# Performance work log

Hardware: AMD Instinct MI355X
Metric: run time of the kernel (lower is better)

## Reference

```python
import jax, jax.numpy as jnp
import numpy as np

N = 100000
E = 800000
D_IN = 64
D_HID = 64
D_OUT = 47


def gcn_conv(x, edge_index, W, b):
    # GCNConv with normalize=False: linear transform then sum-aggregate over edges.
    h = x @ W                              # [N, d_out]
    src, dst = edge_index[0], edge_index[1]
    msg = h[src]                           # [E, d_out] gather
    agg = jax.ops.segment_sum(msg, dst, num_segments=N)  # [N, d_out] scatter-add
    return agg + b


def setup_inputs() -> dict:
    key = jax.random.key(0)
    ks = jax.random.split(key, 8)
    x = jax.random.normal(ks[0], (N, D_IN), dtype=jnp.float32)
    edge_index = jax.random.randint(ks[1], (2, E), 0, N, dtype=jnp.int64)
    # Glorot-ish init for weights, zeros for bias (as in GCNConv.reset_parameters)
    def glorot(k, fan_in, fan_out):
        s = jnp.sqrt(6.0 / (fan_in + fan_out))
        return jax.random.uniform(k, (fan_in, fan_out), jnp.float32, -s, s)
    W1 = glorot(ks[2], D_IN, D_HID)
    b1 = jnp.zeros((D_HID,), jnp.float32)
    W2 = glorot(ks[3], D_HID, D_HID)
    b2 = jnp.zeros((D_HID,), jnp.float32)
    W3 = glorot(ks[4], D_HID, D_OUT)
    b3 = jnp.zeros((D_OUT,), jnp.float32)
    return {"x": x, "edge_index": edge_index,
            "W1": W1, "b1": b1, "W2": W2, "b2": b2, "W3": W3, "b3": b3}


def reference(x, edge_index, W1, b1, W2, b2, W3, b3):
    # Layer 1: conv -> relu (dropout is identity at inference)
    h = jax.nn.relu(gcn_conv(x, edge_index, W1, b1))
    # Layer 2
    h = jax.nn.relu(gcn_conv(h, edge_index, W2, b2))
    # Output layer + log_softmax over classes
    out = gcn_conv(h, edge_index, W3, b3)
    return jax.nn.log_softmax(out, axis=-1)
```

## Files before the change

kernel.cpp:

```cpp
#include <hip/hip_runtime.h>
#include <cmath>


#define B1_EPB 4096
#define BKT_SH 8
#define CHUNK  256
#define PSTRIDE 512

typedef __attribute__((ext_vector_type(8))) short bf8;
typedef __attribute__((ext_vector_type(4))) float f4;

__device__ __forceinline__ unsigned int f2bf(float x) {
  unsigned int u = __float_as_uint(x);
  return (u + 0x7FFFu + ((u >> 16) & 1u)) >> 16;
}
__device__ __forceinline__ float bflo(unsigned int u) { return __uint_as_float(u << 16); }
__device__ __forceinline__ float bfhi(unsigned int u) { return __uint_as_float(u & 0xFFFF0000u); }

__global__ void bhist_cvt_k(const int* __restrict__ dsti, int* __restrict__ part,
                            int ne, const float* __restrict__ x,
                            unsigned short* __restrict__ xb, int n4,
                            int nbkt, int nseg) {
  __shared__ int lh[PSTRIDE];
  const int b = blockIdx.x, t = threadIdx.x;
  if (b < nseg) {
    for (int i = t; i < PSTRIDE; i += 256) lh[i] = 0;
    __syncthreads();
    const int base = b * B1_EPB;
    const int m = min(B1_EPB, ne - base);
    for (int i = t; i < m; i += 256) atomicAdd(&lh[dsti[base + i] >> BKT_SH], 1);
    __syncthreads();
    for (int i = t; i < PSTRIDE; i += 256) part[b * PSTRIDE + i] = lh[i];
  }
  const int gid = b * 256 + t, gst = gridDim.x * 256;
  for (int j = gid; j < n4; j += gst) {
    float4 v = ((const float4*)x)[j];
    ushort4 o;
    o.x = (unsigned short)f2bf(v.x); o.y = (unsigned short)f2bf(v.y);
    o.z = (unsigned short)f2bf(v.z); o.w = (unsigned short)f2bf(v.w);
    ((ushort4*)xb)[j] = o;
  }
}

__global__ void bscan_k(const int* __restrict__ part, int* __restrict__ bbase,
                        int* __restrict__ bcur, int nbkt, int nseg, int ne) {
  __shared__ int sh[512];
  const int t = threadIdx.x;
  int s0 = 0, s1 = 0, s2 = 0, s3 = 0, s4 = 0, s5 = 0, s6 = 0, s7 = 0;
  int b = 0;
  for (; b + 7 < nseg; b += 8) {
    s0 += part[(b + 0) * PSTRIDE + t];
    s1 += part[(b + 1) * PSTRIDE + t];
    s2 += part[(b + 2) * PSTRIDE + t];
    s3 += part[(b + 3) * PSTRIDE + t];
    s4 += part[(b + 4) * PSTRIDE + t];
    s5 += part[(b + 5) * PSTRIDE + t];
    s6 += part[(b + 6) * PSTRIDE + t];
    s7 += part[(b + 7) * PSTRIDE + t];
  }
  for (; b < nseg; ++b) s0 += part[b * PSTRIDE + t];
  const int s = ((s0 + s1) + (s2 + s3)) + ((s4 + s5) + (s6 + s7));
  sh[t] = s; __syncthreads();
  for (int o = 1; o < 512; o <<= 1) {
    int v = (t >= o) ? sh[t - o] : 0; __syncthreads();
    sh[t] += v; __syncthreads();
  }
  if (t < nbkt) { int e = sh[t] - s; bbase[t] = e; bcur[t] = e; }
  if (t == 0) bbase[nbkt] = ne;
}

__global__ void bucket_k(const int* __restrict__ srci, const int* __restrict__ dsti,
                         int* __restrict__ bcur, uint2* __restrict__ ebuf,
                         int ne, int nbkt) {
  __shared__ int lhist[512], lbase[512];
  const int t = threadIdx.x;
  const int base = blockIdx.x * B1_EPB;
  const int m = min(B1_EPB, ne - base);
  for (int i = t; i < nbkt; i += 256) lhist[i] = 0;
  __syncthreads();
  for (int i = t; i < m; i += 256) atomicAdd(&lhist[dsti[base + i] >> BKT_SH], 1);
  __syncthreads();
  for (int i = t; i < nbkt; i += 256) {
    int c = lhist[i];
    lbase[i] = c ? atomicAdd(&bcur[i], c) : 0;
  }
  __syncthreads();
  for (int i = t; i < nbkt; i += 256) lhist[i] = 0;
  __syncthreads();
  for (int i = t; i < m; i += 256) {
    const int s = srci[base + i], d = dsti[base + i];
    const int b = d >> BKT_SH;
    const int p = lbase[b] + atomicAdd(&lhist[b], 1);
    ebuf[p] = make_uint2((unsigned)s, (unsigned)d);
  }
}

__global__ void fillb_k(const uint2* __restrict__ ebuf, const int* __restrict__ bbase,
                        int* __restrict__ row_off, int* __restrict__ ssrc,
                        int n, int ne) {
  __shared__ int lcnt[256], lpre[256], lcur[256];
  const int b = blockIdx.x, t = threadIdx.x;
  const int v0 = b << BKT_SH;
  const int nv = min(1 << BKT_SH, n - v0);
  const int start = bbase[b], end = bbase[b + 1];
  lcnt[t] = 0; __syncthreads();
  for (int i = start + t; i < end; i += 256)
    atomicAdd(&lcnt[ebuf[i].y & ((1 << BKT_SH) - 1)], 1);
  __syncthreads();
  const int x = lcnt[t];
  lpre[t] = x; __syncthreads();
  for (int o = 1; o < 256; o <<= 1) {
    int v = (t >= o) ? lpre[t - o] : 0; __syncthreads();
    lpre[t] += v; __syncthreads();
  }
  const int excl = start + lpre[t] - x;
  lcur[t] = excl;
  if (t < nv) row_off[v0 + t] = excl;
  if (t == 0) row_off[v0 + nv] = end;
  __syncthreads();
  for (int i = start + t; i < end; i += 256) {
    const uint2 e = ebuf[i];
    const int p = atomicAdd(&lcur[e.y & ((1 << BKT_SH) - 1)], 1);
    ssrc[p] = (int)e.x;
  }
}

template <int DOUT, bool LS>
__launch_bounds__(256, 4)
__global__ void fused_k(const unsigned short* __restrict__ in,
                        const int* __restrict__ row_off, const int* __restrict__ ssrc,
                        const float* __restrict__ Wm, const float* __restrict__ bin,
                        void* __restrict__ outp, int n) {
  constexpr int NT = (DOUT + 15) / 16;
  const int lane  = threadIdx.x & 63;
  const int wslot = threadIdx.x >> 6;
  const int quad  = lane >> 4;
  const int f16i  = lane & 15;

  __shared__ char rows_raw[4][16 * 144];
  __shared__ int  sidx[4][CHUNK];
  char* my  = rows_raw[wslot];
  int*  sid = sidx[wslot];

  bf8 bfr[2][NT];
#pragma unroll
  for (int s = 0; s < 2; ++s)
#pragma unroll
    for (int t = 0; t < NT; ++t) {
      const int c = t * 16 + f16i;
#pragma unroll
      for (int j = 0; j < 8; ++j) {
        const int k = s * 32 + quad * 8 + j;
        float wv = (c < DOUT) ? Wm[k * DOUT + c] : 0.f;
        bfr[s][t][j] = (short)f2bf(wv);
      }
    }
  float bc[NT];
#pragma unroll
  for (int t = 0; t < NT; ++t) {
    const int c = t * 16 + f16i;
    bc[t] = (c < DOUT) ? bin[c] : 0.f;
  }

  const uint2* in2 = (const uint2*)in;
  const int wid = (int)((blockIdx.x * blockDim.x + threadIdx.x) >> 6);
  const int nwv = (int)((gridDim.x * blockDim.x) >> 6);
  const int ntiles = (n + 15) >> 4;

  for (int tile = wid; tile < ntiles; tile += nwv) {
    const int v0 = tile << 4;
    const int ro_l = row_off[min(v0 + min(lane, 16), n)];
    const int base     = __shfl(ro_l, 0, 64);
    const int tile_end = __shfl(ro_l, 16, 64);
    int ns[4], nE[4];
#pragma unroll
    for (int r = 0; r < 4; ++r) {
      const int m = quad * 4 + r;
      ns[r] = __shfl(ro_l, m, 64);
      nE[r] = __shfl(ro_l, m + 1, 64);
    }

    float4 accA[4], accB[4];
#pragma unroll
    for (int r = 0; r < 4; ++r) {
      accA[r] = make_float4(0.f, 0.f, 0.f, 0.f);
      accB[r] = make_float4(0.f, 0.f, 0.f, 0.f);
    }

    for (int off = base; off < tile_end; off += CHUNK) {
      const int cend = min(tile_end, off + CHUNK);
      const int nL = cend - off;
#pragma unroll
      for (int k = 0; k < CHUNK / 64; ++k) {
        const int p = off + lane + k * 64;
        if (p < cend) sid[lane + k * 64] = ssrc[p];
      }
      asm volatile("s_waitcnt lgkmcnt(0)" ::: "memory");

#pragma unroll
      for (int r = 0; r < 4; ++r) {
        const int ls = max(ns[r], off), le = min(nE[r], cend);
        for (int c = ls; c < le; c += 8) {
          uint2 q[8];
#pragma unroll
          for (int k = 0; k < 8; ++k) {
            const int lofs = min(c - off + k, nL - 1);
            const int s = sid[lofs];
            q[k] = (c + k < le) ? in2[(size_t)s * 16 + f16i]
                                : make_uint2(0u, 0u);
          }
#pragma unroll
          for (int k = 0; k < 8; k += 2) {
            accA[r].x += bflo(q[k].x); accB[r].x += bflo(q[k + 1].x);
            accA[r].y += bfhi(q[k].x); accB[r].y += bfhi(q[k + 1].x);
            accA[r].z += bflo(q[k].y); accB[r].z += bflo(q[k + 1].y);
            accA[r].w += bfhi(q[k].y); accB[r].w += bfhi(q[k + 1].y);
          }
        }
      }
    }

#pragma unroll
    for (int r = 0; r < 4; ++r) {
      const int m = quad * 4 + r;
      uint2 p;
      p.x = f2bf(accA[r].x + accB[r].x) | (f2bf(accA[r].y + accB[r].y) << 16);
      p.y = f2bf(accA[r].z + accB[r].z) | (f2bf(accA[r].w + accB[r].w) << 16);
      *(uint2*)(my + m * 144 + f16i * 8) = p;
    }
    asm volatile("s_waitcnt lgkmcnt(0)" ::: "memory");

    bf8 a0 = *(const bf8*)(my + f16i * 144 + quad * 16);
    bf8 a1 = *(const bf8*)(my + f16i * 144 + quad * 16 + 64);
    f4 acc[NT];
#pragma unroll
    for (int t = 0; t < NT; ++t) {
      f4 z = {0.f, 0.f, 0.f, 0.f};
      acc[t] = __builtin_amdgcn_mfma_f32_16x16x32_bf16(a0, bfr[0][t], z, 0, 0, 0);
      acc[t] = __builtin_amdgcn_mfma_f32_16x16x32_bf16(a1, bfr[1][t], acc[t], 0, 0, 0);
    }

    if (!LS) {
      unsigned short* ob = (unsigned short*)outp;
#pragma unroll
      for (int t = 0; t < NT; ++t)
#pragma unroll
        for (int j = 0; j < 4; ++j) {
          const int v = v0 + quad * 4 + j;
          if (v < n) {
            float val = acc[t][j] + bc[t];
            ob[(size_t)v * 64 + t * 16 + f16i] =
                (unsigned short)f2bf(fmaxf(val, 0.f));
          }
        }
    } else {
      float* ob = (float*)outp;
      float val[NT][4];
#pragma unroll
      for (int t = 0; t < NT; ++t)
#pragma unroll
        for (int j = 0; j < 4; ++j) val[t][j] = acc[t][j] + bc[t];
#pragma unroll
      for (int j = 0; j < 4; ++j) {
        float mx = -INFINITY;
#pragma unroll
        for (int t = 0; t < NT; ++t)
          if (t * 16 + f16i < DOUT) mx = fmaxf(mx, val[t][j]);
#pragma unroll
        for (int o = 1; o <= 8; o <<= 1) mx = fmaxf(mx, __shfl_xor(mx, o, 64));
        float sm = 0.f;
#pragma unroll
        for (int t = 0; t < NT; ++t)
          if (t * 16 + f16i < DOUT) sm += __expf(val[t][j] - mx);
#pragma unroll
        for (int o = 1; o <= 8; o <<= 1) sm += __shfl_xor(sm, o, 64);
        const float lse = mx + __logf(sm);
        const int v = v0 + quad * 4 + j;
        if (v < n) {
#pragma unroll
          for (int t = 0; t < NT; ++t) {
            const int c = t * 16 + f16i;
            if (c < DOUT) ob[(size_t)v * DOUT + c] = val[t][j] - lse;
          }
        }
      }
    }
  }
}

extern "C" void kernel_launch(void* const* d_in, const int* in_sizes, int n_in,
                              void* d_out, int out_size, void* d_ws, size_t ws_size,
                              hipStream_t stream) {
  const float* x  = (const float*)d_in[0];
  const int*   ei = (const int*)d_in[1];
  const float* W1 = (const float*)d_in[2];
  const float* b1 = (const float*)d_in[3];
  const float* W2 = (const float*)d_in[4];
  const float* b2 = (const float*)d_in[5];
  const float* W3 = (const float*)d_in[6];
  const float* b3 = (const float*)d_in[7];
  float* outp = (float*)d_out;

  const int n  = in_sizes[0] / 64;
  const int ne = in_sizes[1] / 2;
  const int* srci = ei;
  const int* dsti = ei + ne;
  const int nbkt = (n + (1 << BKT_SH) - 1) >> BKT_SH;
  const int nseg = (ne + B1_EPB - 1) / B1_EPB;

  const size_t N64 = (size_t)n * 64;
  unsigned short* xb   = (unsigned short*)d_ws;
  unsigned short* bufA = xb + N64;
  unsigned short* bufB = bufA + N64;
  uint2* ebuf   = (uint2*)(bufB + N64);
  int* row_off  = (int*)(ebuf + ne);
  int* part     = row_off + n + 1;
  int* bbase    = part + nseg * PSTRIDE;
  int* bcur     = bbase + nbkt + 1;
  int* ssrc     = bcur + nbkt;

  const int TB = 256;
  const int fus_blocks = 1568;

  bhist_cvt_k<<<784, TB, 0, stream>>>(dsti, part, ne, x, xb, (int)(N64 / 4), nbkt, nseg);
  bscan_k<<<1, 512, 0, stream>>>(part, bbase, bcur, nbkt, nseg, ne);
  bucket_k<<<nseg, TB, 0, stream>>>(srci, dsti, bcur, ebuf, ne, nbkt);
  fillb_k<<<nbkt, TB, 0, stream>>>(ebuf, bbase, row_off, ssrc, n, ne);

  fused_k<64, false><<<fus_blocks, TB, 0, stream>>>(xb,   row_off, ssrc, W1, b1, bufA, n);
  fused_k<64, false><<<fus_blocks, TB, 0, stream>>>(bufA, row_off, ssrc, W2, b2, bufB, n);
  fused_k<47, true ><<<fus_blocks, TB, 0, stream>>>(bufB, row_off, ssrc, W3, b3, outp, n);
}
```

Baseline: 208.2 us.

## Pack bucket edges into 32-bit words and move MFMA weights to LDS

The bucket pass now stores each edge as a single 32-bit word (source index shifted left 8 bits, with the low 8 bits of the destination), halving the traffic of the edge buffer. The fused layer kernel keeps the bf16 weight matrix in shared memory instead of registers, merges the two accumulator sets into one, and raises the launch bound's minimum blocks per multiprocessor from 4 to 6. The aim is lower register pressure and higher occupancy so more gathers are in flight. The cost is extra LDS reads per tile and a longer dependency chain in the accumulation. The packing also only holds while source indices fit in 24 bits.

```diff
diff --git a/kernel.cpp b/kernel.cpp
--- a/kernel.cpp
+++ b/kernel.cpp
@@ -70,7 +70,7 @@
 }
 
 __global__ void bucket_k(const int* __restrict__ srci, const int* __restrict__ dsti,
-                         int* __restrict__ bcur, uint2* __restrict__ ebuf,
+                         int* __restrict__ bcur, unsigned* __restrict__ ebuf,
                          int ne, int nbkt) {
   __shared__ int lhist[512], lbase[512];
   const int t = threadIdx.x;
@@ -91,11 +91,11 @@
     const int s = srci[base + i], d = dsti[base + i];
     const int b = d >> BKT_SH;
     const int p = lbase[b] + atomicAdd(&lhist[b], 1);
-    ebuf[p] = make_uint2((unsigned)s, (unsigned)d);
-  }
-}
-
-__global__ void fillb_k(const uint2* __restrict__ ebuf, const int* __restrict__ bbase,
+    ebuf[p] = ((unsigned)s << 8) | ((unsigned)d & 255u);
+  }
+}
+
+__global__ void fillb_k(const unsigned* __restrict__ ebuf, const int* __restrict__ bbase,
                         int* __restrict__ row_off, int* __restrict__ ssrc,
                         int n, int ne) {
   __shared__ int lcnt[256], lpre[256], lcur[256];
@@ -105,7 +105,7 @@
   const int start = bbase[b], end = bbase[b + 1];
   lcnt[t] = 0; __syncthreads();
   for (int i = start + t; i < end; i += 256)
-    atomicAdd(&lcnt[ebuf[i].y & ((1 << BKT_SH) - 1)], 1);
+    atomicAdd(&lcnt[ebuf[i] & 255u], 1);
   __syncthreads();
   const int x = lcnt[t];
   lpre[t] = x; __syncthreads();
@@ -119,19 +119,20 @@
   if (t == 0) row_off[v0 + nv] = end;
   __syncthreads();
   for (int i = start + t; i < end; i += 256) {
-    const uint2 e = ebuf[i];
-    const int p = atomicAdd(&lcur[e.y & ((1 << BKT_SH) - 1)], 1);
-    ssrc[p] = (int)e.x;
+    const unsigned e = ebuf[i];
+    const int p = atomicAdd(&lcur[e & 255u], 1);
+    ssrc[p] = (int)(e >> 8);
   }
 }
 
 template <int DOUT, bool LS>
-__launch_bounds__(256, 4)
+__launch_bounds__(256, 6)
 __global__ void fused_k(const unsigned short* __restrict__ in,
                         const int* __restrict__ row_off, const int* __restrict__ ssrc,
                         const float* __restrict__ Wm, const float* __restrict__ bin,
                         void* __restrict__ outp, int n) {
   constexpr int NT = (DOUT + 15) / 16;
+  constexpr int NC = NT * 16;
   const int lane  = threadIdx.x & 63;
   const int wslot = threadIdx.x >> 6;
   const int quad  = lane >> 4;
@@ -139,28 +140,22 @@
 
   __shared__ char rows_raw[4][16 * 144];
   __shared__ int  sidx[4][CHUNK];
+  __shared__ char wlds[NC * 144];
   char* my  = rows_raw[wslot];
   int*  sid = sidx[wslot];
 
-  bf8 bfr[2][NT];
-#pragma unroll
-  for (int s = 0; s < 2; ++s)
-#pragma unroll
-    for (int t = 0; t < NT; ++t) {
-      const int c = t * 16 + f16i;
-#pragma unroll
-      for (int j = 0; j < 8; ++j) {
-        const int k = s * 32 + quad * 8 + j;
-        float wv = (c < DOUT) ? Wm[k * DOUT + c] : 0.f;
-        bfr[s][t][j] = (short)f2bf(wv);
-      }
-    }
+  for (int idx = threadIdx.x; idx < NC * 64; idx += 256) {
+    const int k = idx & 63, c = idx >> 6;
+    const float wv = (c < DOUT) ? Wm[k * DOUT + c] : 0.f;
+    *(unsigned short*)(wlds + c * 144 + k * 2) = (unsigned short)f2bf(wv);
+  }
   float bc[NT];
 #pragma unroll
   for (int t = 0; t < NT; ++t) {
     const int c = t * 16 + f16i;
     bc[t] = (c < DOUT) ? bin[c] : 0.f;
   }
+  __syncthreads();
 
   const uint2* in2 = (const uint2*)in;
   const int wid = (int)((blockIdx.x * blockDim.x + threadIdx.x) >> 6);
@@ -180,12 +175,9 @@
       nE[r] = __shfl(ro_l, m + 1, 64);
     }
 
-    float4 accA[4], accB[4];
-#pragma unroll
-    for (int r = 0; r < 4; ++r) {
-      accA[r] = make_float4(0.f, 0.f, 0.f, 0.f);
-      accB[r] = make_float4(0.f, 0.f, 0.f, 0.f);
-    }
+    float4 accs[4];
+#pragma unroll
+    for (int r = 0; r < 4; ++r) accs[r] = make_float4(0.f, 0.f, 0.f, 0.f);
 
     for (int off = base; off < tile_end; off += CHUNK) {
       const int cend = min(tile_end, off + CHUNK);
@@ -210,11 +202,11 @@
                                 : make_uint2(0u, 0u);
           }
 #pragma unroll
-          for (int k = 0; k < 8; k += 2) {
-            accA[r].x += bflo(q[k].x); accB[r].x += bflo(q[k + 1].x);
-            accA[r].y += bfhi(q[k].x); accB[r].y += bfhi(q[k + 1].x);
-            accA[r].z += bflo(q[k].y); accB[r].z += bflo(q[k + 1].y);
-            accA[r].w += bfhi(q[k].y); accB[r].w += bfhi(q[k + 1].y);
+          for (int k = 0; k < 8; ++k) {
+            accs[r].x += bflo(q[k].x);
+            accs[r].y += bfhi(q[k].x);
+            accs[r].z += bflo(q[k].y);
+            accs[r].w += bfhi(q[k].y);
           }
         }
       }
@@ -224,8 +216,8 @@
     for (int r = 0; r < 4; ++r) {
       const int m = quad * 4 + r;
       uint2 p;
-      p.x = f2bf(accA[r].x + accB[r].x) | (f2bf(accA[r].y + accB[r].y) << 16);
-      p.y = f2bf(accA[r].z + accB[r].z) | (f2bf(accA[r].w + accB[r].w) << 16);
+      p.x = f2bf(accs[r].x) | (f2bf(accs[r].y) << 16);
+      p.y = f2bf(accs[r].z) | (f2bf(accs[r].w) << 16);
       *(uint2*)(my + m * 144 + f16i * 8) = p;
     }
     asm volatile("s_waitcnt lgkmcnt(0)" ::: "memory");
@@ -235,9 +227,12 @@
     f4 acc[NT];
 #pragma unroll
     for (int t = 0; t < NT; ++t) {
+      const char* wrow = wlds + (t * 16 + f16i) * 144 + quad * 16;
+      bf8 b0 = *(const bf8*)(wrow);
+      bf8 b1 = *(const bf8*)(wrow + 64);
       f4 z = {0.f, 0.f, 0.f, 0.f};
-      acc[t] = __builtin_amdgcn_mfma_f32_16x16x32_bf16(a0, bfr[0][t], z, 0, 0, 0);
-      acc[t] = __builtin_amdgcn_mfma_f32_16x16x32_bf16(a1, bfr[1][t], acc[t], 0, 0, 0);
+      acc[t] = __builtin_amdgcn_mfma_f32_16x16x32_bf16(a0, b0, z, 0, 0, 0);
+      acc[t] = __builtin_amdgcn_mfma_f32_16x16x32_bf16(a1, b1, acc[t], 0, 0, 0);
     }
 
     if (!LS) {
@@ -312,7 +307,7 @@
   unsigned short* xb   = (unsigned short*)d_ws;
   unsigned short* bufA = xb + N64;
   unsigned short* bufB = bufA + N64;
-  uint2* ebuf   = (uint2*)(bufB + N64);
+  unsigned* ebuf = (unsigned*)(bufB + N64);
   int* row_off  = (int*)(ebuf + ne);
   int* part     = row_off + n + 1;
   int* bbase    = part + nseg * PSTRIDE;
```

New measurement: 229.5 us. +10.2%, slower.

## Pack bucketed edges into 32-bit words and interleave row gathers in aggregation

Applied to the files above, without the earlier changes.

The bucket pass now stores each edge as a single 32-bit word, holding the source shifted left by 8 with the low 8 bits of the destination, instead of a uint2 pair. This halves the traffic into and out of the temporary edge buffer, but only holds while source ids fit in 24 bits. The aggregation loop now walks all four rows a lane owns together, issuing 4 gathers per row per step (16 in flight) rather than finishing one row before starting the next with 8 gathers. This should hide latency better when row degrees differ, at the cost of masked loads on rows that end early and the loss of the split accumulators.

```diff
diff --git a/kernel.cpp b/kernel.cpp
--- a/kernel.cpp
+++ b/kernel.cpp
@@ -70,7 +70,7 @@
 }
 
 __global__ void bucket_k(const int* __restrict__ srci, const int* __restrict__ dsti,
-                         int* __restrict__ bcur, uint2* __restrict__ ebuf,
+                         int* __restrict__ bcur, unsigned* __restrict__ ebuf,
                          int ne, int nbkt) {
   __shared__ int lhist[512], lbase[512];
   const int t = threadIdx.x;
@@ -91,11 +91,11 @@
     const int s = srci[base + i], d = dsti[base + i];
     const int b = d >> BKT_SH;
     const int p = lbase[b] + atomicAdd(&lhist[b], 1);
-    ebuf[p] = make_uint2((unsigned)s, (unsigned)d);
-  }
-}
-
-__global__ void fillb_k(const uint2* __restrict__ ebuf, const int* __restrict__ bbase,
+    ebuf[p] = ((unsigned)s << 8) | ((unsigned)d & 255u);
+  }
+}
+
+__global__ void fillb_k(const unsigned* __restrict__ ebuf, const int* __restrict__ bbase,
                         int* __restrict__ row_off, int* __restrict__ ssrc,
                         int n, int ne) {
   __shared__ int lcnt[256], lpre[256], lcur[256];
@@ -105,7 +105,7 @@
   const int start = bbase[b], end = bbase[b + 1];
   lcnt[t] = 0; __syncthreads();
   for (int i = start + t; i < end; i += 256)
-    atomicAdd(&lcnt[ebuf[i].y & ((1 << BKT_SH) - 1)], 1);
+    atomicAdd(&lcnt[ebuf[i] & 255u], 1);
   __syncthreads();
   const int x = lcnt[t];
   lpre[t] = x; __syncthreads();
@@ -119,9 +119,9 @@
   if (t == 0) row_off[v0 + nv] = end;
   __syncthreads();
   for (int i = start + t; i < end; i += 256) {
-    const uint2 e = ebuf[i];
-    const int p = atomicAdd(&lcur[e.y & ((1 << BKT_SH) - 1)], 1);
-    ssrc[p] = (int)e.x;
+    const unsigned e = ebuf[i];
+    const int p = atomicAdd(&lcur[e & 255u], 1);
+    ssrc[p] = (int)(e >> 8);
   }
 }
 
@@ -180,12 +180,9 @@
       nE[r] = __shfl(ro_l, m + 1, 64);
     }
 
-    float4 accA[4], accB[4];
-#pragma unroll
-    for (int r = 0; r < 4; ++r) {
-      accA[r] = make_float4(0.f, 0.f, 0.f, 0.f);
-      accB[r] = make_float4(0.f, 0.f, 0.f, 0.f);
-    }
+    float4 accs[4];
+#pragma unroll
+    for (int r = 0; r < 4; ++r) accs[r] = make_float4(0.f, 0.f, 0.f, 0.f);
 
     for (int off = base; off < tile_end; off += CHUNK) {
       const int cend = min(tile_end, off + CHUNK);
@@ -197,25 +194,37 @@
       }
       asm volatile("s_waitcnt lgkmcnt(0)" ::: "memory");
 
+      int cur[4], le[4];
 #pragma unroll
       for (int r = 0; r < 4; ++r) {
-        const int ls = max(ns[r], off), le = min(nE[r], cend);
-        for (int c = ls; c < le; c += 8) {
-          uint2 q[8];
-#pragma unroll
-          for (int k = 0; k < 8; ++k) {
-            const int lofs = min(c - off + k, nL - 1);
-            const int s = sid[lofs];
-            q[k] = (c + k < le) ? in2[(size_t)s * 16 + f16i]
-                                : make_uint2(0u, 0u);
+        cur[r] = max(ns[r], off);
+        le[r]  = min(nE[r], cend);
+      }
+      for (;;) {
+        bool any = (cur[0] < le[0]) | (cur[1] < le[1]) |
+                   (cur[2] < le[2]) | (cur[3] < le[3]);
+        if (!any) break;
+        uint2 q[4][4];
+#pragma unroll
+        for (int r = 0; r < 4; ++r)
+#pragma unroll
+          for (int k = 0; k < 4; ++k) {
+            const int idx  = cur[r] + k;
+            const int lofs = min(idx - off, nL - 1);
+            const int s    = sid[lofs];
+            q[r][k] = (idx < le[r]) ? in2[(size_t)s * 16 + f16i]
+                                    : make_uint2(0u, 0u);
           }
 #pragma unroll
-          for (int k = 0; k < 8; k += 2) {
-            accA[r].x += bflo(q[k].x); accB[r].x += bflo(q[k + 1].x);
-            accA[r].y += bfhi(q[k].x); accB[r].y += bfhi(q[k + 1].x);
-            accA[r].z += bflo(q[k].y); accB[r].z += bflo(q[k + 1].y);
-            accA[r].w += bfhi(q[k].y); accB[r].w += bfhi(q[k + 1].y);
+        for (int r = 0; r < 4; ++r) {
+#pragma unroll
+          for (int k = 0; k < 4; ++k) {
+            accs[r].x += bflo(q[r][k].x);
+            accs[r].y += bfhi(q[r][k].x);
+            accs[r].z += bflo(q[r][k].y);
+            accs[r].w += bfhi(q[r][k].y);
           }
+          cur[r] += 4;
         }
       }
     }
@@ -224,8 +233,8 @@
     for (int r = 0; r < 4; ++r) {
       const int m = quad * 4 + r;
       uint2 p;
-      p.x = f2bf(accA[r].x + accB[r].x) | (f2bf(accA[r].y + accB[r].y) << 16);
-      p.y = f2bf(accA[r].z + accB[r].z) | (f2bf(accA[r].w + accB[r].w) << 16);
+      p.x = f2bf(accs[r].x) | (f2bf(accs[r].y) << 16);
+      p.y = f2bf(accs[r].z) | (f2bf(accs[r].w) << 16);
       *(uint2*)(my + m * 144 + f16i * 8) = p;
     }
     asm volatile("s_waitcnt lgkmcnt(0)" ::: "memory");
@@ -312,7 +321,7 @@
   unsigned short* xb   = (unsigned short*)d_ws;
   unsigned short* bufA = xb + N64;
   unsigned short* bufB = bufA + N64;
-  uint2* ebuf   = (uint2*)(bufB + N64);
+  unsigned* ebuf = (unsigned*)(bufB + N64);
   int* row_off  = (int*)(ebuf + ne);
   int* part     = row_off + n + 1;
   int* bbase    = part + nseg * PSTRIDE;
```

New measurement: 220.8 us. +6.1%, slower.
